# Kernel tuning notes

Hardware: AMD Instinct MI355X
Metric: run time of the kernel (lower is better)

## Reference

```python
import jax, jax.numpy as jnp
import numpy as np

N, F_IN, HID, C, E = 100000, 1024, 16, 64, 3200000
BN_EPS = 1e-5


def setup_inputs() -> dict:
    key = jax.random.key(0)
    ks = jax.random.split(key, 8)
    x = jax.random.normal(ks[0], (N, F_IN), jnp.float32)
    edge_index = jax.random.randint(ks[1], (2, E), 0, N, dtype=jnp.int32)
    w1 = jax.random.normal(ks[2], (F_IN, HID), jnp.float32) / np.float32(np.sqrt(F_IN))
    b1 = jnp.zeros((HID,), jnp.float32)
    w2 = jax.random.normal(ks[3], (HID, C), jnp.float32) / np.float32(np.sqrt(HID))
    b2 = jnp.zeros((C,), jnp.float32)
    mlp_w = jax.random.normal(ks[4], (C, C), jnp.float32) / np.float32(np.sqrt(C))
    mlp_b = jnp.zeros((C,), jnp.float32)
    bn_gamma = jnp.ones((C,), jnp.float32)
    bn_beta = jnp.zeros((C,), jnp.float32)
    # per-node channel weight param, xavier_normal_ init on shape (N, 1)
    xavier_std = np.float32(np.sqrt(2.0 / (N + 1)))
    weight_raw = jax.random.normal(ks[5], (N, 1), jnp.float32) * xavier_std
    return {"x": x, "edge_index": edge_index, "w1": w1, "b1": b1, "w2": w2,
            "b2": b2, "mlp_w": mlp_w, "mlp_b": mlp_b, "bn_gamma": bn_gamma,
            "bn_beta": bn_beta, "weight_raw": weight_raw}


def _gcn_norm(edge_index, n):
    # PyG GCNConv default: add self-loops, norm = deg^-1/2[src] * deg^-1/2[dst]
    loop = jnp.arange(n, dtype=edge_index.dtype)
    src = jnp.concatenate([edge_index[0], loop])
    dst = jnp.concatenate([edge_index[1], loop])
    deg = jax.ops.segment_sum(jnp.ones_like(dst, dtype=jnp.float32), dst, num_segments=n)
    dis = jax.lax.rsqrt(jnp.maximum(deg, 1.0))  # deg >= 1 with self-loops
    norm = dis[src] * dis[dst]
    return src, dst, norm


def _gcn_conv(h, src, dst, norm, w, b, n):
    h = h @ w                              # [N, out] dense transform first
    msg = h[src] * norm[:, None]           # gather + scale per edge
    out = jax.ops.segment_sum(msg, dst, num_segments=n)  # scatter-add
    return out + b


def reference(x, edge_index, w1, b1, w2, b2, mlp_w, mlp_b, bn_gamma, bn_beta, weight_raw):
    n = x.shape[0]
    src, dst, norm = _gcn_norm(edge_index, n)
    h = _gcn_conv(x, src, dst, norm, w1, b1, n)
    h = jax.nn.relu(h)                     # dropout is identity in eval mode
    h = _gcn_conv(h, src, dst, norm, w2, b2, n)
    h = jax.nn.log_softmax(h, axis=1)
    h = jnp.exp(weight_raw) * h            # exp(xavier param) channel weight
    h = h @ mlp_w + mlp_b                  # final MLP (C*1 -> C)
    mean = jnp.mean(h, axis=0)
    var = jnp.mean(jnp.square(h - mean), axis=0)  # biased var, BN training stats
    h = (h - mean) * jax.lax.rsqrt(var + BN_EPS) * bn_gamma + bn_beta
    return jax.nn.log_softmax(h, axis=1)
```

## Files before the change

### kernel.cpp

```cpp
#include <hip/hip_runtime.h>
#include <math.h>

#define NN   100000
#define FIN  1024
#define HIDN 16
#define CCH  64
#define EE   3200000
#define BNEPS 1e-5f
#define NB   ((NN + 255) / 256)
#define NPART 8
#define PSZ  (NN / NPART)

__global__ __launch_bounds__(256) void k_hist(const int* __restrict__ ei,
                                              unsigned* __restrict__ deg) {
  int p = blockIdx.x & 7;
  int blk = blockIdx.x >> 3;
  int nblk = gridDim.x >> 3;
  int lo = p * PSZ, hi = lo + PSZ;
  for (int e = blk * 256 + threadIdx.x; e < EE; e += nblk * 256) {
    int d = ei[EE + e];
    if (d >= lo && d < hi) atomicAdd(&deg[d], 1u);
  }
}

__global__ __launch_bounds__(256) void k_scan_part(const unsigned* __restrict__ deg,
                                                   unsigned* __restrict__ exc,
                                                   unsigned* __restrict__ bsum) {
  __shared__ unsigned s[256];
  int t = threadIdx.x, i = blockIdx.x * 256 + t;
  unsigned v = (i < NN) ? deg[i] : 0u;
  s[t] = v;
  __syncthreads();
#pragma unroll
  for (int off = 1; off < 256; off <<= 1) {
    unsigned u = (t >= off) ? s[t - off] : 0u;
    __syncthreads();
    s[t] += u;
    __syncthreads();
  }
  if (i < NN) exc[i] = s[t] - v;
  if (t == 255) bsum[blockIdx.x] = s[255];
}

__global__ __launch_bounds__(512) void k_scan_boff(const unsigned* __restrict__ bsum,
                                                   unsigned* __restrict__ boff) {
  __shared__ unsigned s[512];
  int t = threadIdx.x;
  unsigned v = (t < NB) ? bsum[t] : 0u;
  s[t] = v;
  __syncthreads();
#pragma unroll
  for (int off = 1; off < 512; off <<= 1) {
    unsigned u = (t >= off) ? s[t - off] : 0u;
    __syncthreads();
    s[t] += u;
    __syncthreads();
  }
  if (t < NB) boff[t] = s[t] - v;
}

__global__ __launch_bounds__(256) void k_scan_final(const unsigned* __restrict__ exc,
                                                    const unsigned* __restrict__ boff,
                                                    const unsigned* __restrict__ deg,
                                                    int* __restrict__ rowptr,
                                                    int* __restrict__ cur,
                                                    float* __restrict__ dis) {
  int i = blockIdx.x * 256 + threadIdx.x;
  if (i < NN) {
    int r = (int)(boff[i >> 8] + exc[i]);
    rowptr[i] = r;
    cur[i] = r;
    dis[i] = rsqrtf((float)(deg[i] + 1u));
  } else if (i == NN) {
    rowptr[NN] = EE;
  }
}

__global__ __launch_bounds__(256) void k_place(const int* __restrict__ ei,
                                               int* __restrict__ cur,
                                               int* __restrict__ perm) {
  int p = blockIdx.x & 7;
  int blk = blockIdx.x >> 3;
  int nblk = gridDim.x >> 3;
  int lo = p * PSZ, hi = lo + PSZ;
  for (int e = blk * 256 + threadIdx.x; e < EE; e += nblk * 256) {
    int d = ei[EE + e];
    if (d >= lo && d < hi) {
      int s = ei[e];
      int slot = atomicAdd(&cur[d], 1);
      perm[slot] = s;
    }
  }
}

#define G1_ROWS_PER_BLOCK 128
__global__ __launch_bounds__(256, 2) void k_gemm1(const float* __restrict__ x,
                                                  const float* __restrict__ w1,
                                                  const float* __restrict__ dis,
                                                  float* __restrict__ xw1s) {
  __shared__ __align__(16) float w1s[1024 * 16];
  const float4* w1v = (const float4*)w1;
  for (int idx = threadIdx.x; idx < 4096; idx += 256) {
    int k = idx >> 2, qj = idx & 3;
    int pq = qj ^ ((k >> 1) & 3);
    *(float4*)&w1s[(k << 4) + (pq << 2)] = w1v[idx];
  }
  __syncthreads();

  const int lane = threadIdx.x & 63;
  const int wave = threadIdx.x >> 6;
  const int sw = (lane >> 1) & 3;
  const int wave_row0 = blockIdx.x * G1_ROWS_PER_BLOCK + wave * 32;

  for (int g = 0; g < 8; ++g) {
    int row0 = wave_row0 + g * 4;
    if (row0 >= NN) break;
    int r0 = row0;
    int r1 = min(row0 + 1, NN - 1);
    int r2 = min(row0 + 2, NN - 1);
    int r3 = min(row0 + 3, NN - 1);

    const float* p0 = x + (size_t)r0 * FIN + lane;
    const float* p1 = x + (size_t)r1 * FIN + lane;
    const float* p2 = x + (size_t)r2 * FIN + lane;
    const float* p3 = x + (size_t)r3 * FIN + lane;

    float xa[16], xb[16], xc[16], xd[16];
#pragma unroll
    for (int i = 0; i < 16; ++i) {
      xa[i] = __builtin_nontemporal_load(p0 + i * 64);
      xb[i] = __builtin_nontemporal_load(p1 + i * 64);
      xc[i] = __builtin_nontemporal_load(p2 + i * 64);
      xd[i] = __builtin_nontemporal_load(p3 + i * 64);
    }

    float acc[64];
#pragma unroll
    for (int t = 0; t < 64; ++t) acc[t] = 0.0f;

#pragma unroll
    for (int i = 0; i < 16; ++i) {
      const float* wr = &w1s[(i * 64 + lane) << 4];
      float xv0 = xa[i], xv1 = xb[i], xv2 = xc[i], xv3 = xd[i];
#pragma unroll
      for (int q = 0; q < 4; ++q) {
        float4 wq = *(const float4*)(wr + ((q ^ sw) << 2));
        int b = q * 4;
        acc[b + 0]      += xv0 * wq.x;
        acc[b + 1]      += xv0 * wq.y;
        acc[b + 2]      += xv0 * wq.z;
        acc[b + 3]      += xv0 * wq.w;
        acc[16 + b + 0] += xv1 * wq.x;
        acc[16 + b + 1] += xv1 * wq.y;
        acc[16 + b + 2] += xv1 * wq.z;
        acc[16 + b + 3] += xv1 * wq.w;
        acc[32 + b + 0] += xv2 * wq.x;
        acc[32 + b + 1] += xv2 * wq.y;
        acc[32 + b + 2] += xv2 * wq.z;
        acc[32 + b + 3] += xv2 * wq.w;
        acc[48 + b + 0] += xv3 * wq.x;
        acc[48 + b + 1] += xv3 * wq.y;
        acc[48 + b + 2] += xv3 * wq.z;
        acc[48 + b + 3] += xv3 * wq.w;
      }
    }

#pragma unroll
    for (int o = 32; o >= 1; o >>= 1) {
      bool up = (lane & o) != 0;
#pragma unroll
      for (int t = 0; t < o; ++t) {
        float send = up ? acc[t] : acc[t + o];
        float recv = __shfl_xor(send, o, 64);
        float keep = up ? acc[t + o] : acc[t];
        acc[t] = keep + recv;
      }
    }

    int grow = row0 + (lane >> 4);
    if (grow < NN) xw1s[grow * HIDN + (lane & 15)] = acc[0] * dis[grow];
  }
}

template <int MODE>
__global__ __launch_bounds__(256) void k_agg(const int* __restrict__ rowptr,
                                             const int* __restrict__ perm,
                                             const float* __restrict__ dis,
                                             const float* __restrict__ sfs,
                                             const float* __restrict__ b1,
                                             float* __restrict__ out) {
  int g = blockIdx.x * 4 + (threadIdx.x >> 6);
  if (g >= NN) return;
  int lane = threadIdx.x & 63;
  int eo = lane >> 4;
  int j = lane & 15;
  int beg = rowptr[g], end = rowptr[g + 1];
  float acc0 = 0.0f, acc1 = 0.0f;
  int e = beg + eo;
  for (; e + 4 < end; e += 8) {
    int s0 = perm[e];
    int s1 = perm[e + 4];
    acc0 += sfs[(size_t)s0 * HIDN + j];
    acc1 += sfs[(size_t)s1 * HIDN + j];
  }
  if (e < end) acc0 += sfs[(size_t)perm[e] * HIDN + j];
  float acc = acc0 + acc1;
  acc += __shfl_xor(acc, 16, 64);
  acc += __shfl_xor(acc, 32, 64);
  if (eo == 0) {
    float di = dis[g];
    float v = di * (acc + sfs[(size_t)g * HIDN + j]);
    if (MODE == 0)
      out[(size_t)g * HIDN + j] = fmaxf(v + b1[j], 0.0f) * di;
    else
      out[(size_t)g * HIDN + j] = v;
  }
}

__global__ __launch_bounds__(256) void k_fuse2(const float* __restrict__ agg2,
                                               const float* __restrict__ w2,
                                               const float* __restrict__ b2,
                                               const float* __restrict__ mlpw,
                                               const float* __restrict__ mlpb,
                                               const float* __restrict__ wraw,
                                               float* __restrict__ out,
                                               double* __restrict__ gsum,
                                               double* __restrict__ gsq) {
  __shared__ __align__(16) float2 w2p[8 * CCH];
  __shared__ __align__(16) float2 mlpp[32 * CCH];
  __shared__ __align__(16) float avbuf[4][HIDN];
  __shared__ __align__(16) float gbuf[4][CCH];
  __shared__ double reds[256];
  __shared__ double redq[256];
  for (int idx = threadIdx.x; idx < 8 * CCH; idx += 256) {
    int k2 = idx >> 6, j = idx & 63;
    w2p[idx] = make_float2(w2[(2 * k2) * CCH + j], w2[(2 * k2 + 1) * CCH + j]);
  }
  for (int idx = threadIdx.x; idx < 32 * CCH; idx += 256) {
    int c2 = idx >> 6, j = idx & 63;
    mlpp[idx] = make_float2(mlpw[(2 * c2) * CCH + j], mlpw[(2 * c2 + 1) * CCH + j]);
  }
  __syncthreads();

  const int lane = threadIdx.x & 63;
  const int wave = threadIdx.x >> 6;
  const int j = lane;
  const float b2j = b2[j];
  const float mbj = mlpb[j];
  const int gw = blockIdx.x * 4 + wave;
  const int nw = gridDim.x * 4;

  double sum = 0.0, sq = 0.0;
  for (int i = gw; i < NN; i += nw) {
    float av = agg2[(size_t)i * HIDN + (lane & 15)];
    if (lane < HIDN) avbuf[wave][lane] = av;

    float2 h2p = make_float2(0.0f, 0.0f);
#pragma unroll
    for (int k2 = 0; k2 < 8; ++k2) {
      float2 a = *(const float2*)&avbuf[wave][2 * k2];
      float2 wv = w2p[k2 * CCH + j];
      h2p.x = fmaf(a.x, wv.x, h2p.x);
      h2p.y = fmaf(a.y, wv.y, h2p.y);
    }
    float h2 = h2p.x + h2p.y + b2j;

    float mx = h2;
#pragma unroll
    for (int o = 32; o >= 1; o >>= 1) mx = fmaxf(mx, __shfl_xor(mx, o, 64));
    float ex = __expf(h2 - mx);
    float se = ex;
#pragma unroll
    for (int o = 32; o >= 1; o >>= 1) se += __shfl_xor(se, o, 64);
    float lsm = h2 - mx - __logf(se);

    float gg = __expf(wraw[i]) * lsm;
    gbuf[wave][j] = gg;

    float2 mp = make_float2(0.0f, 0.0f);
#pragma unroll
    for (int c2 = 0; c2 < 32; ++c2) {
      float2 gv = *(const float2*)&gbuf[wave][2 * c2];
      float2 wv = mlpp[c2 * CCH + j];
      mp.x = fmaf(gv.x, wv.x, mp.x);
      mp.y = fmaf(gv.y, wv.y, mp.y);
    }
    float m = mp.x + mp.y + mbj;

    out[(size_t)i * CCH + j] = m;
    sum += (double)m;
    sq = fma((double)m, (double)m, sq);
  }

  reds[threadIdx.x] = sum;
  redq[threadIdx.x] = sq;
  __syncthreads();
  if (threadIdx.x < 64) {
    double s = reds[threadIdx.x] + reds[threadIdx.x + 64] +
               reds[threadIdx.x + 128] + reds[threadIdx.x + 192];
    double q = redq[threadIdx.x] + redq[threadIdx.x + 64] +
               redq[threadIdx.x + 128] + redq[threadIdx.x + 192];
    atomicAdd(&gsum[threadIdx.x], s);
    atomicAdd(&gsq[threadIdx.x], q);
  }
}

__global__ void k_stats(const double* __restrict__ gsum,
                        const double* __restrict__ gsq,
                        const float* __restrict__ gamma,
                        const float* __restrict__ beta,
                        float* __restrict__ bnp) {
  int j = threadIdx.x;
  if (j >= CCH) return;
  const double inv_n = 1.0 / (double)NN;
  double mean = gsum[j] * inv_n;
  double var = gsq[j] * inv_n - mean * mean;
  float sc = (float)(rsqrt(var + (double)BNEPS)) * gamma[j];
  bnp[j] = (float)mean;
  bnp[CCH + j] = sc;
  bnp[2 * CCH + j] = beta[j];
}

__global__ __launch_bounds__(256) void k_out(float* __restrict__ out,
                                             const float* __restrict__ bnp) {
  const int lane = threadIdx.x & 63;
  const int wave = threadIdx.x >> 6;
  const int j = lane;
  const float mean = bnp[j];
  const float sc = bnp[CCH + j];
  const float bt = bnp[2 * CCH + j];
  const int gw = blockIdx.x * 4 + wave;
  const int nw = gridDim.x * 4;
  for (int i = gw; i < NN; i += nw) {
    float m = out[(size_t)i * CCH + j];
    float y = fmaf(m - mean, sc, bt);
    float mx = y;
#pragma unroll
    for (int o = 32; o >= 1; o >>= 1) mx = fmaxf(mx, __shfl_xor(mx, o, 64));
    float ex = __expf(y - mx);
    float se = ex;
#pragma unroll
    for (int o = 32; o >= 1; o >>= 1) se += __shfl_xor(se, o, 64);
    out[(size_t)i * CCH + j] = y - mx - __logf(se);
  }
}

extern "C" void kernel_launch(void* const* d_in, const int* in_sizes, int n_in,
                              void* d_out, int out_size, void* d_ws, size_t ws_size,
                              hipStream_t stream) {
  const float* x     = (const float*)d_in[0];
  const int*   ei    = (const int*)d_in[1];
  const float* w1    = (const float*)d_in[2];
  const float* b1    = (const float*)d_in[3];
  const float* w2    = (const float*)d_in[4];
  const float* b2    = (const float*)d_in[5];
  const float* mlpw  = (const float*)d_in[6];
  const float* mlpb  = (const float*)d_in[7];
  const float* gamma = (const float*)d_in[8];
  const float* beta  = (const float*)d_in[9];
  const float* wraw  = (const float*)d_in[10];
  float* out = (float*)d_out;

  char* w = (char*)d_ws;
  size_t off = 0;
  auto take = [&](size_t bytes) -> void* {
    void* p = w + off;
    off = (off + bytes + 255) & ~(size_t)255;
    return p;
  };
  unsigned* deg    = (unsigned*)take((size_t)NN * 4);
  float*    dis    = (float*)take((size_t)NN * 4);
  unsigned* exc    = (unsigned*)take((size_t)NN * 4);
  unsigned* bsum   = (unsigned*)take((size_t)NB * 4);
  unsigned* boff   = (unsigned*)take((size_t)NB * 4);
  int*      rowptr = (int*)take((size_t)(NN + 1) * 4);
  int*      cur    = (int*)take((size_t)NN * 4);
  int*      perm   = (int*)take((size_t)EE * 4);
  float*    xw1s   = (float*)take((size_t)NN * HIDN * 4);
  float*    rh1s   = (float*)take((size_t)NN * HIDN * 4);
  float*    agg2   = (float*)take((size_t)NN * HIDN * 4);
  double*   gsum   = (double*)take(CCH * 8);
  double*   gsq    = (double*)take(CCH * 8);
  float*    bnp    = (float*)take(3 * CCH * 4);
  (void)ws_size; (void)n_in; (void)in_sizes; (void)out_size;

  hipMemsetAsync(deg, 0, (size_t)NN * 4, stream);
  hipMemsetAsync(gsum, 0, CCH * 8, stream);
  hipMemsetAsync(gsq, 0, CCH * 8, stream);

  k_hist<<<2048, 256, 0, stream>>>(ei, deg);
  k_scan_part<<<NB, 256, 0, stream>>>(deg, exc, bsum);
  k_scan_boff<<<1, 512, 0, stream>>>(bsum, boff);
  k_scan_final<<<(NN + 256) / 256 + 1, 256, 0, stream>>>(exc, boff, deg, rowptr, cur, dis);
  k_place<<<2048, 256, 0, stream>>>(ei, cur, perm);

  k_gemm1<<<(NN + G1_ROWS_PER_BLOCK - 1) / G1_ROWS_PER_BLOCK, 256, 0, stream>>>(
      x, w1, dis, xw1s);
  k_agg<0><<<(NN + 3) / 4, 256, 0, stream>>>(rowptr, perm, dis, xw1s, b1, rh1s);
  k_agg<1><<<(NN + 3) / 4, 256, 0, stream>>>(rowptr, perm, dis, rh1s, b1, agg2);
  k_fuse2<<<2048, 256, 0, stream>>>(agg2, w2, b2, mlpw, mlpb, wraw, out, gsum, gsq);
  k_stats<<<1, 64, 0, stream>>>(gsum, gsq, gamma, beta, bnp);
  k_out<<<1024, 256, 0, stream>>>(out, bnp);
}
```

Before: 593.6 us.

## Fuse second aggregation with W2/log-softmax/MLP and split BN stats into separate pass

Merges the second-layer neighbor aggregation into the dense W2, log-softmax, channel weight and MLP kernel, so the agg2 intermediate buffer and one launch go away. The fused kernel now runs one node per wave with 25000 blocks, and each block reloads the W2 and MLP weights into shared memory, which adds per-block setup cost. BN sum and sum-of-squares move to a new kernel that rereads the full 100000x64 output from global memory, adding about 25 MB of traffic.

```diff
diff --git a/kernel.cpp b/kernel.cpp
--- a/kernel.cpp
+++ b/kernel.cpp
@@ -182,13 +182,12 @@
   }
 }
 
-template <int MODE>
-__global__ __launch_bounds__(256) void k_agg(const int* __restrict__ rowptr,
-                                             const int* __restrict__ perm,
-                                             const float* __restrict__ dis,
-                                             const float* __restrict__ sfs,
-                                             const float* __restrict__ b1,
-                                             float* __restrict__ out) {
+__global__ __launch_bounds__(256) void k_agg1(const int* __restrict__ rowptr,
+                                              const int* __restrict__ perm,
+                                              const float* __restrict__ dis,
+                                              const float* __restrict__ sfs,
+                                              const float* __restrict__ b1,
+                                              float* __restrict__ out) {
   int g = blockIdx.x * 4 + (threadIdx.x >> 6);
   if (g >= NN) return;
   int lane = threadIdx.x & 63;
@@ -210,28 +209,24 @@
   if (eo == 0) {
     float di = dis[g];
     float v = di * (acc + sfs[(size_t)g * HIDN + j]);
-    if (MODE == 0)
-      out[(size_t)g * HIDN + j] = fmaxf(v + b1[j], 0.0f) * di;
-    else
-      out[(size_t)g * HIDN + j] = v;
-  }
-}
-
-__global__ __launch_bounds__(256) void k_fuse2(const float* __restrict__ agg2,
-                                               const float* __restrict__ w2,
-                                               const float* __restrict__ b2,
-                                               const float* __restrict__ mlpw,
-                                               const float* __restrict__ mlpb,
-                                               const float* __restrict__ wraw,
-                                               float* __restrict__ out,
-                                               double* __restrict__ gsum,
-                                               double* __restrict__ gsq) {
+    out[(size_t)g * HIDN + j] = fmaxf(v + b1[j], 0.0f) * di;
+  }
+}
+
+__global__ __launch_bounds__(256) void k_aggfuse(const int* __restrict__ rowptr,
+                                                 const int* __restrict__ perm,
+                                                 const float* __restrict__ dis,
+                                                 const float* __restrict__ sfs,
+                                                 const float* __restrict__ w2,
+                                                 const float* __restrict__ b2,
+                                                 const float* __restrict__ mlpw,
+                                                 const float* __restrict__ mlpb,
+                                                 const float* __restrict__ wraw,
+                                                 float* __restrict__ out) {
   __shared__ __align__(16) float2 w2p[8 * CCH];
   __shared__ __align__(16) float2 mlpp[32 * CCH];
   __shared__ __align__(16) float avbuf[4][HIDN];
   __shared__ __align__(16) float gbuf[4][CCH];
-  __shared__ double reds[256];
-  __shared__ double redq[256];
   for (int idx = threadIdx.x; idx < 8 * CCH; idx += 256) {
     int k2 = idx >> 6, j = idx & 63;
     w2p[idx] = make_float2(w2[(2 * k2) * CCH + j], w2[(2 * k2 + 1) * CCH + j]);
@@ -242,66 +237,87 @@
   }
   __syncthreads();
 
+  const int g = blockIdx.x * 4 + (threadIdx.x >> 6);
+  if (g >= NN) return;
   const int lane = threadIdx.x & 63;
   const int wave = threadIdx.x >> 6;
+  const int eo = lane >> 4;
+  const int jc = lane & 15;
   const int j = lane;
-  const float b2j = b2[j];
-  const float mbj = mlpb[j];
-  const int gw = blockIdx.x * 4 + wave;
-  const int nw = gridDim.x * 4;
-
-  double sum = 0.0, sq = 0.0;
-  for (int i = gw; i < NN; i += nw) {
-    float av = agg2[(size_t)i * HIDN + (lane & 15)];
-    if (lane < HIDN) avbuf[wave][lane] = av;
-
-    float2 h2p = make_float2(0.0f, 0.0f);
-#pragma unroll
-    for (int k2 = 0; k2 < 8; ++k2) {
-      float2 a = *(const float2*)&avbuf[wave][2 * k2];
-      float2 wv = w2p[k2 * CCH + j];
-      h2p.x = fmaf(a.x, wv.x, h2p.x);
-      h2p.y = fmaf(a.y, wv.y, h2p.y);
-    }
-    float h2 = h2p.x + h2p.y + b2j;
-
-    float mx = h2;
-#pragma unroll
-    for (int o = 32; o >= 1; o >>= 1) mx = fmaxf(mx, __shfl_xor(mx, o, 64));
-    float ex = __expf(h2 - mx);
-    float se = ex;
-#pragma unroll
-    for (int o = 32; o >= 1; o >>= 1) se += __shfl_xor(se, o, 64);
-    float lsm = h2 - mx - __logf(se);
-
-    float gg = __expf(wraw[i]) * lsm;
-    gbuf[wave][j] = gg;
-
-    float2 mp = make_float2(0.0f, 0.0f);
-#pragma unroll
-    for (int c2 = 0; c2 < 32; ++c2) {
-      float2 gv = *(const float2*)&gbuf[wave][2 * c2];
-      float2 wv = mlpp[c2 * CCH + j];
-      mp.x = fmaf(gv.x, wv.x, mp.x);
-      mp.y = fmaf(gv.y, wv.y, mp.y);
-    }
-    float m = mp.x + mp.y + mbj;
-
-    out[(size_t)i * CCH + j] = m;
-    sum += (double)m;
-    sq = fma((double)m, (double)m, sq);
-  }
-
-  reds[threadIdx.x] = sum;
-  redq[threadIdx.x] = sq;
+
+  int beg = rowptr[g], end = rowptr[g + 1];
+  float acc0 = 0.0f, acc1 = 0.0f;
+  int e = beg + eo;
+  for (; e + 4 < end; e += 8) {
+    int s0 = perm[e];
+    int s1 = perm[e + 4];
+    acc0 += sfs[(size_t)s0 * HIDN + jc];
+    acc1 += sfs[(size_t)s1 * HIDN + jc];
+  }
+  if (e < end) acc0 += sfs[(size_t)perm[e] * HIDN + jc];
+  float acc = acc0 + acc1;
+  acc += __shfl_xor(acc, 16, 64);
+  acc += __shfl_xor(acc, 32, 64);
+  float di = dis[g];
+  float av = di * (acc + sfs[(size_t)g * HIDN + jc]);
+  if (lane < HIDN) avbuf[wave][lane] = av;
+
+  float2 h2p = make_float2(0.0f, 0.0f);
+#pragma unroll
+  for (int k2 = 0; k2 < 8; ++k2) {
+    float2 a = *(const float2*)&avbuf[wave][2 * k2];
+    float2 wv = w2p[k2 * CCH + j];
+    h2p.x = fmaf(a.x, wv.x, h2p.x);
+    h2p.y = fmaf(a.y, wv.y, h2p.y);
+  }
+  float h2 = h2p.x + h2p.y + b2[j];
+
+  float mx = h2;
+#pragma unroll
+  for (int o = 32; o >= 1; o >>= 1) mx = fmaxf(mx, __shfl_xor(mx, o, 64));
+  float ex = __expf(h2 - mx);
+  float se = ex;
+#pragma unroll
+  for (int o = 32; o >= 1; o >>= 1) se += __shfl_xor(se, o, 64);
+  float lsm = h2 - mx - __logf(se);
+
+  float gg = __expf(wraw[g]) * lsm;
+  gbuf[wave][j] = gg;
+
+  float2 mp = make_float2(0.0f, 0.0f);
+#pragma unroll
+  for (int c2 = 0; c2 < 32; ++c2) {
+    float2 gv = *(const float2*)&gbuf[wave][2 * c2];
+    float2 wv = mlpp[c2 * CCH + j];
+    mp.x = fmaf(gv.x, wv.x, mp.x);
+    mp.y = fmaf(gv.y, wv.y, mp.y);
+  }
+  out[(size_t)g * CCH + j] = mp.x + mp.y + mlpb[j];
+}
+
+__global__ __launch_bounds__(256) void k_bnstats(const float* __restrict__ out,
+                                                 double* __restrict__ gsum,
+                                                 double* __restrict__ gsq) {
+  __shared__ double reds[256];
+  __shared__ double redq[256];
+  const int lane = threadIdx.x & 63;
+  const int wave = threadIdx.x >> 6;
+  double s = 0.0, q = 0.0;
+  for (int i = blockIdx.x * 4 + wave; i < NN; i += gridDim.x * 4) {
+    float m = out[(size_t)i * CCH + lane];
+    s += (double)m;
+    q = fma((double)m, (double)m, q);
+  }
+  reds[threadIdx.x] = s;
+  redq[threadIdx.x] = q;
   __syncthreads();
   if (threadIdx.x < 64) {
-    double s = reds[threadIdx.x] + reds[threadIdx.x + 64] +
-               reds[threadIdx.x + 128] + reds[threadIdx.x + 192];
-    double q = redq[threadIdx.x] + redq[threadIdx.x + 64] +
-               redq[threadIdx.x + 128] + redq[threadIdx.x + 192];
-    atomicAdd(&gsum[threadIdx.x], s);
-    atomicAdd(&gsq[threadIdx.x], q);
+    double ss = reds[threadIdx.x] + reds[threadIdx.x + 64] +
+                reds[threadIdx.x + 128] + reds[threadIdx.x + 192];
+    double qq = redq[threadIdx.x] + redq[threadIdx.x + 64] +
+                redq[threadIdx.x + 128] + redq[threadIdx.x + 192];
+    atomicAdd(&gsum[threadIdx.x], ss);
+    atomicAdd(&gsq[threadIdx.x], qq);
   }
 }
 
@@ -378,7 +394,6 @@
   int*      perm   = (int*)take((size_t)EE * 4);
   float*    xw1s   = (float*)take((size_t)NN * HIDN * 4);
   float*    rh1s   = (float*)take((size_t)NN * HIDN * 4);
-  float*    agg2   = (float*)take((size_t)NN * HIDN * 4);
   double*   gsum   = (double*)take(CCH * 8);
   double*   gsq    = (double*)take(CCH * 8);
   float*    bnp    = (float*)take(3 * CCH * 4);
@@ -396,9 +411,11 @@
 
   k_gemm1<<<(NN + G1_ROWS_PER_BLOCK - 1) / G1_ROWS_PER_BLOCK, 256, 0, stream>>>(
       x, w1, dis, xw1s);
-  k_agg<0><<<(NN + 3) / 4, 256, 0, stream>>>(rowptr, perm, dis, xw1s, b1, rh1s);
-  k_agg<1><<<(NN + 3) / 4, 256, 0, stream>>>(rowptr, perm, dis, rh1s, b1, agg2);
-  k_fuse2<<<2048, 256, 0, stream>>>(agg2, w2, b2, mlpw, mlpb, wraw, out, gsum, gsq);
+  k_agg1<<<(NN + 3) / 4, 256, 0, stream>>>(rowptr, perm, dis, xw1s, b1, rh1s);
+  k_aggfuse<<<(NN + 3) / 4, 256, 0, stream>>>(rowptr, perm, dis, rh1s, w2, b2,
+                                              mlpw, mlpb, wraw, out);
+
+  k_bnstats<<<256, 256, 0, stream>>>(out, gsum, gsq);
   k_stats<<<1, 64, 0, stream>>>(gsum, gsq, gamma, beta, bnp);
   k_out<<<1024, 256, 0, stream>>>(out, bnp);
 }
```

New measurement: 606.9 us. +2.2%, slower.
